# Performance work log

Hardware: AMD Instinct MI355X
Metric: run time of the kernel (lower is better)

The kernel has to match this reference:

```python
import jax, jax.numpy as jnp
import numpy as np

N = 50000          # nodes
E = 800000         # directed edges (before self loops)
H = 2              # attention heads
NEG_SLOPE = 0.2    # PyG GATv2 default
EPS = 1e-5         # GraphNorm eps
DIMS = [(3, 64), (64, 64), (64, 64)]


def _gatv2_layer(x, Wl, Wr, att, b, src, dst):
    # x: [N, din]; Wl, Wr: [din, H*C]; att: [H, C]; b: [C]
    n = x.shape[0]
    h, c = att.shape
    xl = (x @ Wl).reshape(n, h, c)   # source-side transform
    xr = (x @ Wr).reshape(n, h, c)   # target-side transform
    # edge-wise GATv2 score: a . leaky_relu(xl[j] + xr[i])
    e = jax.nn.leaky_relu(xl[src] + xr[dst], NEG_SLOPE)      # [E, H, C]
    logit = jnp.einsum('ehc,hc->eh', e, att)                 # [E, H]
    # segment softmax over incoming edges of each target node
    m = jax.ops.segment_max(logit, dst, num_segments=n)      # [N, H]
    a = jnp.exp(logit - m[dst])
    z = jax.ops.segment_sum(a, dst, num_segments=n)
    alpha = a / z[dst]                                       # [E, H]
    out = jax.ops.segment_sum(alpha[:, :, None] * xl[src], dst, num_segments=n)  # [N, H, C]
    return out.mean(axis=1) + b                              # concat=False -> head mean


def _graph_norm(x, w, b, ms):
    # single-graph GraphNorm: x -> w * (x - ms*mean) / sqrt(var + eps) + b
    mu = x.mean(axis=0)
    o = x - ms * mu
    var = (o * o).mean(axis=0)
    return w * o * jax.lax.rsqrt(var + EPS) + b


def setup_inputs() -> dict:
    key = jax.random.key(0)
    ks = jax.random.split(key, 2 + 3 * len(DIMS))
    inp = {
        'x': jax.random.normal(ks[0], (N, 3), dtype=jnp.float32),
        'edge_index': jax.random.randint(ks[1], (2, E), 0, N, dtype=jnp.int32),
    }
    for i, (din, dout) in enumerate(DIMS, start=1):
        k0, k1, k2 = ks[2 + 3 * (i - 1):2 + 3 * i]
        s_in = np.float32(1.0 / np.sqrt(din))
        s_att = np.float32(1.0 / np.sqrt(dout))
        inp[f'Wl{i}'] = jax.random.normal(k0, (din, H * dout), dtype=jnp.float32) * s_in
        inp[f'Wr{i}'] = jax.random.normal(k1, (din, H * dout), dtype=jnp.float32) * s_in
        inp[f'att{i}'] = jax.random.normal(k2, (H, dout), dtype=jnp.float32) * s_att
        inp[f'b{i}'] = jnp.zeros((dout,), dtype=jnp.float32)
        inp[f'gw{i}'] = jnp.ones((dout,), dtype=jnp.float32)
        inp[f'gb{i}'] = jnp.zeros((dout,), dtype=jnp.float32)
        inp[f'gm{i}'] = jnp.ones((dout,), dtype=jnp.float32)
    return inp


def reference(x, edge_index,
              Wl1, Wr1, att1, b1, gw1, gb1, gm1,
              Wl2, Wr2, att2, b2, gw2, gb2, gm2,
              Wl3, Wr3, att3, b3, gw3, gb3, gm3):
    n = x.shape[0]
    loop = jnp.arange(n, dtype=edge_index.dtype)
    src = jnp.concatenate([edge_index[0], loop])  # add_self_loops=True
    dst = jnp.concatenate([edge_index[1], loop])
    layers = [(Wl1, Wr1, att1, b1, gw1, gb1, gm1),
              (Wl2, Wr2, att2, b2, gw2, gb2, gm2),
              (Wl3, Wr3, att3, b3, gw3, gb3, gm3)]
    for Wl, Wr, att, b, gw, gb, gm in layers:
        x = _gatv2_layer(x, Wl, Wr, att, b, src, dst)
        x = jax.nn.relu(_graph_norm(x, gw, gb, gm))
    return x
```

## Files before the change

### kernel.cpp

```cpp
#include <hip/hip_runtime.h>
#include <math.h>

#define NN 50000
#define NE 800000
#define TE (NE + NN)
#define HC 128
#define NEG_SLOPE 0.2f
#define EPSV 1e-5f
#define NBUCK 64
#define GGRID 782
#define WTB 128
#define ZB 52
#define ZERO_N4 18644

typedef __attribute__((ext_vector_type(8))) short bf16x8;
typedef __attribute__((ext_vector_type(4))) float f32x4;
union BfU { uint4 u; bf16x8 b; };

__device__ __forceinline__ unsigned short f2bf(float x) {
    unsigned u = __float_as_uint(x);
    unsigned r = (u + 0x7fff + ((u >> 16) & 1)) >> 16;
    return (unsigned short)r;
}


__global__ __launch_bounds__(256) void count_k(const int* __restrict__ dst,
                                               int* __restrict__ cnt,
                                               int* __restrict__ rank) {
    int e = blockIdx.x * 256 + threadIdx.x;
    if (e >= TE) return;
    int d = (e < NE) ? dst[e] : (e - NE);
    rank[e] = atomicAdd(&cnt[d], 1);
}

__global__ __launch_bounds__(1024) void scan1_k(const int* __restrict__ cnt,
                                                int* __restrict__ excl,
                                                int* __restrict__ aux) {
    __shared__ int wsum[16];
    int tid = threadIdx.x;
    int gid = blockIdx.x * 1024 + tid;
    int lane = tid & 63, wid = tid >> 6;
    int v = (gid < NN) ? cnt[gid] : 0;
    int x = v;
#pragma unroll
    for (int off = 1; off < 64; off <<= 1) {
        int t = __shfl_up(x, off, 64);
        if (lane >= off) x += t;
    }
    if (lane == 63) wsum[wid] = x;
    __syncthreads();
    if (wid == 0 && lane < 16) {
        int y = wsum[lane];
#pragma unroll
        for (int off = 1; off < 16; off <<= 1) {
            int t = __shfl_up(y, off, 64);
            if (lane >= off) y += t;
        }
        wsum[lane] = y;
    }
    __syncthreads();
    int base = (wid > 0) ? wsum[wid - 1] : 0;
    int incl = base + x;
    if (gid < NN) excl[gid] = incl - v;
    if (tid == 1023) aux[blockIdx.x] = incl;
}

__global__ __launch_bounds__(256) void scatter_k(const int* __restrict__ srcp,
                                                 const int* __restrict__ dstp,
                                                 const int* __restrict__ excl,
                                                 const int* __restrict__ aux,
                                                 const int* __restrict__ rank,
                                                 int* __restrict__ row_ptr,
                                                 int* __restrict__ col,
                                                 int nblk) {
    __shared__ int auxs[64];
    if (threadIdx.x < 64) {
        int lane = threadIdx.x;
        int v = (lane < nblk) ? aux[lane] : 0;
        int x = v;
#pragma unroll
        for (int off = 1; off < 64; off <<= 1) {
            int t = __shfl_up(x, off, 64);
            if (lane >= off) x += t;
        }
        auxs[lane] = x - v;
    }
    __syncthreads();
    int e = blockIdx.x * 256 + threadIdx.x;
    if (e >= TE) return;
    if (e <= NN) row_ptr[e] = (e == NN) ? TE : excl[e] + auxs[e >> 10];
    int s, d;
    if (e < NE) { s = srcp[e]; d = dstp[e]; } else { s = e - NE; d = s; }
    col[excl[d] + auxs[d >> 10] + rank[e]] = s << 8;
}

__device__ __forceinline__ void store_xlp(char* xlp, int row, int c0, const float* a) {
    unsigned hsel = (unsigned)c0 >> 6;
    unsigned dd = (unsigned)c0 & 31;
    unsigned sub = (c0 & 32) ? 2u : 0u;
    char* q = xlp + (size_t)row * 256 + hsel * 128 + 4 * dd + sub;
#pragma unroll
    for (int j = 0; j < 4; ++j)
        *(unsigned short*)(q + 4 * j) = f2bf(a[j]);
}


__global__ __launch_bounds__(256) void init_k(const float* __restrict__ x,
                                              const float* __restrict__ Wl1,
                                              const float* __restrict__ Wr1,
                                              char* __restrict__ xlp,
                                              char* __restrict__ xrp,
                                              const float* __restrict__ Wl2,
                                              const float* __restrict__ Wr2,
                                              const float* __restrict__ Wl3,
                                              const float* __restrict__ Wr3,
                                              unsigned short* __restrict__ wt2,
                                              unsigned short* __restrict__ wt3,
                                              float4* __restrict__ zero4) {
    __shared__ float xs[32][72];
    __shared__ float ws[32][260];
    int b = blockIdx.x;
    int tid = threadIdx.x;

    if (b >= GGRID) {
        if (b < GGRID + WTB) {
            int idx = (b - GGRID) * 256 + tid;
            int l = idx >> 14;
            int rem = idx & 16383;
            int k = rem >> 8;
            int c = rem & 255;
            const float* W = (l == 0) ? (c < 128 ? Wl2 : Wr2) : (c < 128 ? Wl3 : Wr3);
            float v = W[k * 128 + (c & 127)];
            unsigned short* wt = (l == 0) ? wt2 : wt3;
            wt[c * 64 + k] = f2bf(v);
        } else {
            float4 zv; zv.x = zv.y = zv.z = zv.w = 0.f;
            for (int i = (b - GGRID - WTB) * 256 + tid; i < ZERO_N4; i += ZB * 256)
                zero4[i] = zv;
        }
        return;
    }

    int row0 = b * 64;
    int row_t = (tid >> 5) * 8;
    int c0 = (tid & 31) * 4;
    const int K = 3;

    float acc0[8][4];
    float acc1[8][4];
#pragma unroll
    for (int i = 0; i < 8; ++i)
#pragma unroll
        for (int j = 0; j < 4; ++j) { acc0[i][j] = 0.f; acc1[i][j] = 0.f; }

    for (int i = tid; i < 64 * K; i += 256) {
        int r = i / K;
        int k = i - r * K;
        int row = row0 + r;
        xs[k][r] = (row < NN) ? x[(size_t)row * K + k] : 0.f;
    }
    for (int i = tid; i < K * 64; i += 256) {
        int k = i >> 6;
        int cq = i & 63;
        const float* srcp = (cq < 32) ? &Wl1[(size_t)k * 128 + cq * 4]
                                      : &Wr1[(size_t)k * 128 + (cq - 32) * 4];
        float4 v = *(const float4*)srcp;
        *(float4*)&ws[k][cq * 4] = v;
    }
    __syncthreads();
    for (int k = 0; k < K; ++k) {
        float4 a0 = *(float4*)&xs[k][row_t];
        float4 a1 = *(float4*)&xs[k][row_t + 4];
        float4 b0 = *(float4*)&ws[k][c0];
        float4 b1 = *(float4*)&ws[k][c0 + 128];
        float av[8] = {a0.x, a0.y, a0.z, a0.w, a1.x, a1.y, a1.z, a1.w};
        float bl[4] = {b0.x, b0.y, b0.z, b0.w};
        float br[4] = {b1.x, b1.y, b1.z, b1.w};
#pragma unroll
        for (int i = 0; i < 8; ++i)
#pragma unroll
            for (int j = 0; j < 4; ++j) {
                acc0[i][j] += av[i] * bl[j];
                acc1[i][j] += av[i] * br[j];
            }
    }
#pragma unroll
    for (int i = 0; i < 8; ++i) {
        int row = row0 + row_t + i;
        if (row < NN) {
            store_xlp(xlp, row, c0, acc0[i]);
            store_xlp(xrp, row, c0, acc1[i]);
        }
    }
}

__device__ __forceinline__ void reduce_stats(const float* __restrict__ stats,
                                             const float* __restrict__ gw,
                                             const float* __restrict__ gb,
                                             const float* __restrict__ gm,
                                             float (*part)[128],
                                             float* __restrict__ cf_out) {
    int tid = threadIdx.x;
    int w = tid >> 6;
    int lane = tid & 63;
    float s = 0.f, s2 = 0.f;
    for (int b = 16 * w; b < 16 * w + 16; ++b) {
        s += stats[b * 128 + lane];
        s2 += stats[b * 128 + 64 + lane];
    }
    part[w][lane] = s;
    part[w][64 + lane] = s2;
    __syncthreads();
    if (tid < 64) {
        int c = tid;
        float sum = (part[0][c] + part[1][c]) + (part[2][c] + part[3][c]);
        float sum2 = (part[0][64 + c] + part[1][64 + c]) + (part[2][64 + c] + part[3][64 + c]);
        float inv_n = 1.f / (float)NN;
        float mu = sum * inv_n;
        float ex2 = sum2 * inv_n;
        float g = gm[c];
        float var = ex2 - 2.f * g * mu * mu + g * g * mu * mu;
        float rs = rsqrtf(var + EPSV);
        cf_out[c] = gw[c] * rs;
        cf_out[64 + c] = gb[c] - gw[c] * rs * g * mu;
    }
    __syncthreads();
}


__global__ __launch_bounds__(256) void gemm_mfma(const unsigned* __restrict__ hbf,
                                                 const float* __restrict__ stats,
                                                 const float* __restrict__ gw,
                                                 const float* __restrict__ gb,
                                                 const float* __restrict__ gm,
                                                 const unsigned short* __restrict__ wt,
                                                 char* __restrict__ xlp,
                                                 char* __restrict__ xrp,
                                                 int n) {
    __shared__ unsigned short xs[64][72];
    __shared__ float part[4][128];
    __shared__ float cfS[128];
    int tid = threadIdx.x;
    int row0 = blockIdx.x * 64;

    reduce_stats(stats, gw, gb, gm, part, cfS);

    {
        int r = tid >> 2;
        int q = tid & 3;
        int row = row0 + r;
        unsigned pk[8];
        if (row < n) {
            const unsigned* hp = hbf + (size_t)row * 32 + (q & 1) * 16;
            uint4 u0 = *(const uint4*)(hp + 0);
            uint4 u1 = *(const uint4*)(hp + 4);
            uint4 u2 = *(const uint4*)(hp + 8);
            uint4 u3 = *(const uint4*)(hp + 12);
            unsigned hv[16] = {u0.x, u0.y, u0.z, u0.w, u1.x, u1.y, u1.z, u1.w,
                               u2.x, u2.y, u2.z, u2.w, u3.x, u3.y, u3.z, u3.w};
            bool hi = (q >> 1) != 0;
#pragma unroll
            for (int i = 0; i < 4; ++i) {
                float4 v;
                v.x = hi ? __uint_as_float(hv[4 * i + 0] & 0xffff0000u) : __uint_as_float(hv[4 * i + 0] << 16);
                v.y = hi ? __uint_as_float(hv[4 * i + 1] & 0xffff0000u) : __uint_as_float(hv[4 * i + 1] << 16);
                v.z = hi ? __uint_as_float(hv[4 * i + 2] & 0xffff0000u) : __uint_as_float(hv[4 * i + 2] << 16);
                v.w = hi ? __uint_as_float(hv[4 * i + 3] & 0xffff0000u) : __uint_as_float(hv[4 * i + 3] << 16);
                float4 cw = *(const float4*)&cfS[q * 16 + 4 * i];
                float4 cb = *(const float4*)&cfS[64 + q * 16 + 4 * i];
                float r0 = fmaxf(fmaf(cw.x, v.x, cb.x), 0.f);
                float r1 = fmaxf(fmaf(cw.y, v.y, cb.y), 0.f);
                float r2 = fmaxf(fmaf(cw.z, v.z, cb.z), 0.f);
                float r3 = fmaxf(fmaf(cw.w, v.w, cb.w), 0.f);
                pk[2 * i]     = (unsigned)f2bf(r0) | ((unsigned)f2bf(r1) << 16);
                pk[2 * i + 1] = (unsigned)f2bf(r2) | ((unsigned)f2bf(r3) << 16);
            }
        } else {
#pragma unroll
            for (int i = 0; i < 8; ++i) pk[i] = 0;
        }
        uint4* dst = (uint4*)&xs[r][q * 16];
        dst[0] = make_uint4(pk[0], pk[1], pk[2], pk[3]);
        dst[1] = make_uint4(pk[4], pk[5], pk[6], pk[7]);
    }
    __syncthreads();

    int w = tid >> 6;
    int lane = tid & 63;
    int m = lane & 15;
    int quad = lane >> 4;

    BfU a0, a1;
    a0.u = *(const uint4*)&xs[16 * w + m][quad * 8];
    a1.u = *(const uint4*)&xs[16 * w + m][32 + quad * 8];

    const char* wtb = (const char*)wt + (size_t)(m * 128 + quad * 16);

    f32x4 acc[16];
#pragma unroll
    for (int c = 0; c < 16; ++c) acc[c] = (f32x4){0.f, 0.f, 0.f, 0.f};
#pragma unroll
    for (int c = 0; c < 16; ++c) {
        BfU b0, b1;
        b0.u = *(const uint4*)(wtb + c * 2048);
        b1.u = *(const uint4*)(wtb + c * 2048 + 64);
        acc[c] = __builtin_amdgcn_mfma_f32_16x16x32_bf16(a0.b, b0.b, acc[c], 0, 0, 0);
        acc[c] = __builtin_amdgcn_mfma_f32_16x16x32_bf16(a1.b, b1.b, acc[c], 0, 0, 0);
    }

    int rbase = row0 + 16 * w + quad * 4;
#pragma unroll
    for (int pi = 0; pi < 4; ++pi) {
        int c = (pi & 1) + (pi >> 1) * 4;
        int head = pi >> 1;
        int dd = (pi & 1) * 16 + m;
#pragma unroll
        for (int r = 0; r < 4; ++r) {
            int row = rbase + r;
            if (row < n) {
                unsigned vl = (unsigned)f2bf(acc[c][r]) | ((unsigned)f2bf(acc[c + 2][r]) << 16);
                unsigned vr = (unsigned)f2bf(acc[c + 8][r]) | ((unsigned)f2bf(acc[c + 10][r]) << 16);
                *(unsigned*)(xlp + (size_t)row * 256 + head * 128 + 4 * dd) = vl;
                *(unsigned*)(xrp + (size_t)row * 256 + head * 128 + 4 * dd) = vr;
            }
        }
    }
}


__device__ __forceinline__ void unpack8(uint4 q, float* l) {
    l[0] = __uint_as_float(q.x << 16);
    l[1] = __uint_as_float(q.x & 0xffff0000u);
    l[2] = __uint_as_float(q.y << 16);
    l[3] = __uint_as_float(q.y & 0xffff0000u);
    l[4] = __uint_as_float(q.z << 16);
    l[5] = __uint_as_float(q.z & 0xffff0000u);
    l[6] = __uint_as_float(q.w << 16);
    l[7] = __uint_as_float(q.w & 0xffff0000u);
}

__device__ __forceinline__ float logit_part(const float* l, const float* xv, const float* av) {
    float u1 = 0.f, u2 = 0.f;
#pragma unroll
    for (int k = 0; k < 8; ++k) {
        float t = l[k] + xv[k];
        u1 = fmaf(av[k], t, u1);
        u2 = fmaf(av[k], fabsf(t), u2);
    }
    return fmaf(0.6f, u1, 0.4f * u2);
}

__device__ __forceinline__ float head_reduce(float w) {
    w += __shfl_xor(w, 1, 64);
    w += __shfl_xor(w, 2, 64);
    w += __shfl_xor(w, 4, 64);
    return w;
}

__device__ __forceinline__ void attn_pair(const char* __restrict__ xlp, int lp16,
                                          int off0, int off1, bool v0, bool v1,
                                          const float* xv, const float* av,
                                          float* o, float& zacc) {
    uint4 q0 = *(const uint4*)(xlp + (unsigned)(off0 + lp16));
    uint4 q1 = *(const uint4*)(xlp + (unsigned)(off1 + lp16));
    float l0[8], l1[8];
    unpack8(q0, l0);
    unpack8(q1, l1);
    float w0 = head_reduce(logit_part(l0, xv, av));
    float w1 = head_reduce(logit_part(l1, xv, av));
    float e0 = __expf(w0);
    float e1 = __expf(w1);
    if (!v0) e0 = 0.f;
    if (!v1) e1 = 0.f;
    zacc += e0 + e1;
#pragma unroll
    for (int k = 0; k < 8; ++k) o[k] = fmaf(e1, l1[k], fmaf(e0, l0[k], o[k]));
}

__device__ __forceinline__ void attn_quad(const char* __restrict__ xlp, int lp16,
                                          int off0, int off1, int off2, int off3,
                                          const float* xv, const float* av,
                                          float* o, float& zacc) {
    uint4 q0 = *(const uint4*)(xlp + (unsigned)(off0 + lp16));
    uint4 q1 = *(const uint4*)(xlp + (unsigned)(off1 + lp16));
    uint4 q2 = *(const uint4*)(xlp + (unsigned)(off2 + lp16));
    uint4 q3 = *(const uint4*)(xlp + (unsigned)(off3 + lp16));
    float l0[8], l1[8], l2[8], l3[8];
    unpack8(q0, l0);
    unpack8(q1, l1);
    unpack8(q2, l2);
    unpack8(q3, l3);
    float w0 = head_reduce(logit_part(l0, xv, av));
    float w1 = head_reduce(logit_part(l1, xv, av));
    float w2 = head_reduce(logit_part(l2, xv, av));
    float w3 = head_reduce(logit_part(l3, xv, av));
    float e0 = __expf(w0);
    float e1 = __expf(w1);
    float e2 = __expf(w2);
    float e3 = __expf(w3);
    zacc += (e0 + e1) + (e2 + e3);
#pragma unroll
    for (int k = 0; k < 8; ++k)
        o[k] = fmaf(e3, l3[k], fmaf(e2, l2[k], fmaf(e1, l1[k], fmaf(e0, l0[k], o[k]))));
}

__global__ __launch_bounds__(256) void attn_k(const char* __restrict__ xlp,
                                              const char* __restrict__ xrp,
                                              const float* __restrict__ att,
                                              const float* __restrict__ bias,
                                              const int* __restrict__ row_ptr,
                                              const int* __restrict__ coloff,
                                              unsigned* __restrict__ hout,
                                              float* __restrict__ stats) {
    __shared__ float sb[4][64];
    int tid = threadIdx.x;
    int lane = tid & 63;
    int wv = tid >> 6;
    int node = blockIdx.x * 4 + wv;
    int t16 = lane & 15;
    int slot = (lane >> 4) * 2;
    int head = t16 >> 3;
    int dd = (t16 & 7) * 4;
    int lp16 = t16 * 16;
    int cbase = head * 64 + dd;

    float xv[8];
    unpack8(*(const uint4*)(xrp + ((size_t)node << 8) + lp16), xv);
    float4 a0 = *(const float4*)(att + cbase);
    float4 a1 = *(const float4*)(att + cbase + 32);
    float av[8] = {a0.x, a1.x, a0.y, a1.y, a0.z, a1.z, a0.w, a1.w};

    float o[8];
#pragma unroll
    for (int k = 0; k < 8; ++k) o[k] = 0.f;
    float zacc = 0.f;

    int beg = __builtin_amdgcn_readfirstlane(row_ptr[node]);
    int end = __builtin_amdgcn_readfirstlane(row_ptr[node + 1]);

    int idx = beg;
    for (; idx + 16 <= end; idx += 16) {
        int off0 = coloff[idx + slot];
        int off1 = coloff[idx + slot + 1];
        int off2 = coloff[idx + 8 + slot];
        int off3 = coloff[idx + 8 + slot + 1];
        attn_quad(xlp, lp16, off0, off1, off2, off3, xv, av, o, zacc);
    }
    if (idx + 8 <= end) {
        int off0 = coloff[idx + slot];
        int off1 = coloff[idx + slot + 1];
        attn_pair(xlp, lp16, off0, off1, true, true, xv, av, o, zacc);
        idx += 8;
    }
    if (idx < end) {
        int e1 = end - 1;
        int i0 = idx + slot, i1 = idx + slot + 1;
        int off0 = coloff[min(i0, e1)];
        int off1 = coloff[min(i1, e1)];
        attn_pair(xlp, lp16, off0, off1, i0 < end, i1 < end, xv, av, o, zacc);
    }

    float z = zacc + __shfl_xor(zacc, 16, 64);
    z += __shfl_xor(z, 32, 64);
    float zi = 1.0f / z;
    float r[8];
#pragma unroll
    for (int k = 0; k < 8; ++k) {
        float v = o[k] + __shfl_xor(o[k], 16, 64);
        v += __shfl_xor(v, 32, 64);
        v *= zi;
        float p = __shfl_xor(v, 8, 64);
        r[k] = 0.5f * (v + p);
    }
    if (lane < 8) {
        float4 b0 = *(const float4*)(bias + dd);
        float4 b1 = *(const float4*)(bias + dd + 32);
        float rl0 = r[0] + b0.x, rl1 = r[2] + b0.y, rl2 = r[4] + b0.z, rl3 = r[6] + b0.w;
        float rh0 = r[1] + b1.x, rh1 = r[3] + b1.y, rh2 = r[5] + b1.z, rh3 = r[7] + b1.w;
        unsigned pk0 = (unsigned)f2bf(rl0) | ((unsigned)f2bf(rh0) << 16);
        unsigned pk1 = (unsigned)f2bf(rl1) | ((unsigned)f2bf(rh1) << 16);
        unsigned pk2 = (unsigned)f2bf(rl2) | ((unsigned)f2bf(rh2) << 16);
        unsigned pk3 = (unsigned)f2bf(rl3) | ((unsigned)f2bf(rh3) << 16);
        *(uint4*)&hout[(size_t)node * 32 + dd] = make_uint4(pk0, pk1, pk2, pk3);
        *(float4*)&sb[wv][dd] = make_float4(rl0, rl1, rl2, rl3);
        *(float4*)&sb[wv][dd + 32] = make_float4(rh0, rh1, rh2, rh3);
    }
    __syncthreads();
    if (tid < 64) {
        int c = tid;
        float v0 = sb[0][c], v1 = sb[1][c], v2 = sb[2][c], v3 = sb[3][c];
        float s = (v0 + v1) + (v2 + v3);
        float s2 = fmaf(v0, v0, v1 * v1) + fmaf(v2, v2, v3 * v3);
        float* bkt = stats + (size_t)(blockIdx.x & (NBUCK - 1)) * 128;
        atomicAdd(&bkt[c], s);
        atomicAdd(&bkt[64 + c], s2);
    }
}


__global__ __launch_bounds__(256) void apply_k(const unsigned* __restrict__ h,
                                               const float* __restrict__ stats,
                                               const float* __restrict__ gw,
                                               const float* __restrict__ gb,
                                               const float* __restrict__ gm,
                                               float* __restrict__ y) {
    __shared__ float part[4][128];
    __shared__ float cfS[128];
    reduce_stats(stats, gw, gb, gm, part, cfS);

    int i = blockIdx.x * 256 + threadIdx.x;
    if (i >= NN * 8) return;
    int node = i >> 3;
    int j = (i & 7) * 4;
    uint4 u = *(const uint4*)(h + (size_t)node * 32 + j);
    float4 lo, hi;
    lo.x = __uint_as_float(u.x << 16); hi.x = __uint_as_float(u.x & 0xffff0000u);
    lo.y = __uint_as_float(u.y << 16); hi.y = __uint_as_float(u.y & 0xffff0000u);
    lo.z = __uint_as_float(u.z << 16); hi.z = __uint_as_float(u.z & 0xffff0000u);
    lo.w = __uint_as_float(u.w << 16); hi.w = __uint_as_float(u.w & 0xffff0000u);
    float4 cwl = *(const float4*)&cfS[j];
    float4 cbl = *(const float4*)&cfS[64 + j];
    float4 cwh = *(const float4*)&cfS[32 + j];
    float4 cbh = *(const float4*)&cfS[96 + j];
    float4 rl, rh;
    rl.x = fmaxf(fmaf(cwl.x, lo.x, cbl.x), 0.f);
    rl.y = fmaxf(fmaf(cwl.y, lo.y, cbl.y), 0.f);
    rl.z = fmaxf(fmaf(cwl.z, lo.z, cbl.z), 0.f);
    rl.w = fmaxf(fmaf(cwl.w, lo.w, cbl.w), 0.f);
    rh.x = fmaxf(fmaf(cwh.x, hi.x, cbh.x), 0.f);
    rh.y = fmaxf(fmaf(cwh.y, hi.y, cbh.y), 0.f);
    rh.z = fmaxf(fmaf(cwh.z, hi.z, cbh.z), 0.f);
    rh.w = fmaxf(fmaf(cwh.w, hi.w, cbh.w), 0.f);
    *(float4*)&y[(size_t)node * 64 + j] = rl;
    *(float4*)&y[(size_t)node * 64 + 32 + j] = rh;
}


extern "C" void kernel_launch(void* const* d_in, const int* in_sizes, int n_in,
                              void* d_out, int out_size, void* d_ws, size_t ws_size,
                              hipStream_t stream) {
    const float* x0 = (const float*)d_in[0];
    const int* ei = (const int*)d_in[1];
    const int* srcp = ei;
    const int* dstp = ei + NE;

    const float* Wl[3], *Wr[3], *att[3], *bv[3], *gw[3], *gb[3], *gm[3];
    for (int l = 0; l < 3; ++l) {
        int base = 2 + 7 * l;
        Wl[l] = (const float*)d_in[base + 0];
        Wr[l] = (const float*)d_in[base + 1];
        att[l] = (const float*)d_in[base + 2];
        bv[l] = (const float*)d_in[base + 3];
        gw[l] = (const float*)d_in[base + 4];
        gb[l] = (const float*)d_in[base + 5];
        gm[l] = (const float*)d_in[base + 6];
    }

    char* p = (char*)d_ws;
    auto take = [&](size_t bytes) -> void* {
        void* r = (void*)p;
        p += (bytes + 255) & ~(size_t)255;
        return r;
    };
    char* xlp = (char*)take((size_t)NN * 256);
    char* xrp = (char*)take((size_t)NN * 256);
    unsigned* hb = (unsigned*)take((size_t)NN * 32 * 4);
    char* zr = (char*)take(298304);
    float* stats = (float*)zr;
    int* cnt = (int*)(zr + 98304);
    int* excl = (int*)take((size_t)NN * 4);
    int* row_ptr = (int*)take((size_t)(NN + 1) * 4);
    int* rank = (int*)take((size_t)TE * 4);
    int* col = (int*)take((size_t)TE * 4);
    int* aux = (int*)take(64 * 4);
    unsigned short* wt2 = (unsigned short*)take(16384 * 2);
    unsigned short* wt3 = (unsigned short*)take(16384 * 2);

    int nblk = (NN + 1023) / 1024;
    int egrid = (TE + 255) / 256;

    init_k<<<GGRID + WTB + ZB, 256, 0, stream>>>(x0, Wl[0], Wr[0], xlp, xrp,
                                                 Wl[1], Wr[1], Wl[2], Wr[2],
                                                 wt2, wt3, (float4*)zr);
    count_k<<<egrid, 256, 0, stream>>>(dstp, cnt, rank);
    scan1_k<<<nblk, 1024, 0, stream>>>(cnt, excl, aux);
    scatter_k<<<egrid, 256, 0, stream>>>(srcp, dstp, excl, aux, rank, row_ptr, col, nblk);

    int ggrid = (NN + 63) / 64;
    int agrid = NN / 4;
    for (int l = 0; l < 3; ++l) {
        if (l > 0)
            gemm_mfma<<<ggrid, 256, 0, stream>>>(hb, stats + (size_t)(l - 1) * NBUCK * 128,
                                                 gw[l - 1], gb[l - 1], gm[l - 1],
                                                 (l == 1) ? wt2 : wt3, xlp, xrp, NN);
        attn_k<<<agrid, 256, 0, stream>>>(xlp, xrp, att[l], bv[l], row_ptr, col, hb,
                                          stats + (size_t)l * NBUCK * 128);
    }
    apply_k<<<(NN * 8 + 255) / 256, 256, 0, stream>>>(hb, stats + (size_t)2 * NBUCK * 128,
                                                      gw[2], gb[2], gm[2], (float*)d_out);
}
```

Baseline: 358.1 us.

## Remap attention lanes to 8 per edge with DPP reductions and prefetched offsets

```diff
diff --git a/kernel.cpp b/kernel.cpp
--- a/kernel.cpp
+++ b/kernel.cpp
@@ -328,80 +328,43 @@
 }
 
 
-__device__ __forceinline__ void unpack8(uint4 q, float* l) {
-    l[0] = __uint_as_float(q.x << 16);
-    l[1] = __uint_as_float(q.x & 0xffff0000u);
-    l[2] = __uint_as_float(q.y << 16);
-    l[3] = __uint_as_float(q.y & 0xffff0000u);
-    l[4] = __uint_as_float(q.z << 16);
-    l[5] = __uint_as_float(q.z & 0xffff0000u);
-    l[6] = __uint_as_float(q.w << 16);
-    l[7] = __uint_as_float(q.w & 0xffff0000u);
-}
-
-__device__ __forceinline__ float logit_part(const float* l, const float* xv, const float* av) {
+__device__ __forceinline__ float quad_reduce(float x) {
+    x += __int_as_float(__builtin_amdgcn_mov_dpp(__float_as_int(x), 0xB1, 0xF, 0xF, true));
+    x += __int_as_float(__builtin_amdgcn_mov_dpp(__float_as_int(x), 0x4E, 0xF, 0xF, true));
+    return x;
+}
+
+__device__ __forceinline__ float ror8_add(float x) {
+    return x + __int_as_float(__builtin_amdgcn_mov_dpp(__float_as_int(x), 0x128, 0xF, 0xF, true));
+}
+
+__device__ __forceinline__ void unpack16(uint4 q0, uint4 q1, float* l) {
+    unsigned u[8] = {q0.x, q0.y, q0.z, q0.w, q1.x, q1.y, q1.z, q1.w};
+#pragma unroll
+    for (int j = 0; j < 8; ++j) {
+        l[2 * j]     = __uint_as_float(u[j] << 16);
+        l[2 * j + 1] = __uint_as_float(u[j] & 0xffff0000u);
+    }
+}
+
+__device__ __forceinline__ void edge_proc(uint4 q0, uint4 q1, bool valid,
+                                          const float* xv, const float* av,
+                                          float* o, float& zacc) {
+    float l[16];
+    unpack16(q0, q1, l);
     float u1 = 0.f, u2 = 0.f;
 #pragma unroll
-    for (int k = 0; k < 8; ++k) {
+    for (int k = 0; k < 16; ++k) {
         float t = l[k] + xv[k];
         u1 = fmaf(av[k], t, u1);
         u2 = fmaf(av[k], fabsf(t), u2);
     }
-    return fmaf(0.6f, u1, 0.4f * u2);
-}
-
-__device__ __forceinline__ float head_reduce(float w) {
-    w += __shfl_xor(w, 1, 64);
-    w += __shfl_xor(w, 2, 64);
-    w += __shfl_xor(w, 4, 64);
-    return w;
-}
-
-__device__ __forceinline__ void attn_pair(const char* __restrict__ xlp, int lp16,
-                                          int off0, int off1, bool v0, bool v1,
-                                          const float* xv, const float* av,
-                                          float* o, float& zacc) {
-    uint4 q0 = *(const uint4*)(xlp + (unsigned)(off0 + lp16));
-    uint4 q1 = *(const uint4*)(xlp + (unsigned)(off1 + lp16));
-    float l0[8], l1[8];
-    unpack8(q0, l0);
-    unpack8(q1, l1);
-    float w0 = head_reduce(logit_part(l0, xv, av));
-    float w1 = head_reduce(logit_part(l1, xv, av));
-    float e0 = __expf(w0);
-    float e1 = __expf(w1);
-    if (!v0) e0 = 0.f;
-    if (!v1) e1 = 0.f;
-    zacc += e0 + e1;
-#pragma unroll
-    for (int k = 0; k < 8; ++k) o[k] = fmaf(e1, l1[k], fmaf(e0, l0[k], o[k]));
-}
-
-__device__ __forceinline__ void attn_quad(const char* __restrict__ xlp, int lp16,
-                                          int off0, int off1, int off2, int off3,
-                                          const float* xv, const float* av,
-                                          float* o, float& zacc) {
-    uint4 q0 = *(const uint4*)(xlp + (unsigned)(off0 + lp16));
-    uint4 q1 = *(const uint4*)(xlp + (unsigned)(off1 + lp16));
-    uint4 q2 = *(const uint4*)(xlp + (unsigned)(off2 + lp16));
-    uint4 q3 = *(const uint4*)(xlp + (unsigned)(off3 + lp16));
-    float l0[8], l1[8], l2[8], l3[8];
-    unpack8(q0, l0);
-    unpack8(q1, l1);
-    unpack8(q2, l2);
-    unpack8(q3, l3);
-    float w0 = head_reduce(logit_part(l0, xv, av));
-    float w1 = head_reduce(logit_part(l1, xv, av));
-    float w2 = head_reduce(logit_part(l2, xv, av));
-    float w3 = head_reduce(logit_part(l3, xv, av));
-    float e0 = __expf(w0);
-    float e1 = __expf(w1);
-    float e2 = __expf(w2);
-    float e3 = __expf(w3);
-    zacc += (e0 + e1) + (e2 + e3);
-#pragma unroll
-    for (int k = 0; k < 8; ++k)
-        o[k] = fmaf(e3, l3[k], fmaf(e2, l2[k], fmaf(e1, l1[k], fmaf(e0, l0[k], o[k]))));
+    float w = quad_reduce(fmaf(0.6f, u1, 0.4f * u2));
+    float e = __expf(w);
+    if (!valid) e = 0.f;
+    zacc += e;
+#pragma unroll
+    for (int k = 0; k < 16; ++k) o[k] = fmaf(e, l[k], o[k]);
 }
 
 __global__ __launch_bounds__(256) void attn_k(const char* __restrict__ xlp,
@@ -417,73 +380,111 @@
     int lane = tid & 63;
     int wv = tid >> 6;
     int node = blockIdx.x * 4 + wv;
-    int t16 = lane & 15;
-    int slot = (lane >> 4) * 2;
-    int head = t16 >> 3;
-    int dd = (t16 & 7) * 4;
-    int lp16 = t16 * 16;
-    int cbase = head * 64 + dd;
-
-    float xv[8];
-    unpack8(*(const uint4*)(xrp + ((size_t)node << 8) + lp16), xv);
-    float4 a0 = *(const float4*)(att + cbase);
-    float4 a1 = *(const float4*)(att + cbase + 32);
-    float av[8] = {a0.x, a1.x, a0.y, a1.y, a0.z, a1.z, a0.w, a1.w};
-
-    float o[8];
-#pragma unroll
-    for (int k = 0; k < 8; ++k) o[k] = 0.f;
+    int g = lane >> 3;
+    int t8 = lane & 7;
+    int b32 = t8 * 32;
+    int hd = t8 >> 2;
+    int dd = (t8 & 3) * 8;
+
+    float xv[16];
+    {
+        const char* xq = xrp + ((size_t)node << 8) + b32;
+        unpack16(*(const uint4*)xq, *(const uint4*)(xq + 16), xv);
+    }
+    float av[16];
+    {
+        int base = hd * 64 + dd;
+        float4 a0 = *(const float4*)(att + base);
+        float4 a1 = *(const float4*)(att + base + 4);
+        float4 c0 = *(const float4*)(att + base + 32);
+        float4 c1 = *(const float4*)(att + base + 36);
+        av[0] = a0.x;  av[1] = c0.x;  av[2] = a0.y;  av[3] = c0.y;
+        av[4] = a0.z;  av[5] = c0.z;  av[6] = a0.w;  av[7] = c0.w;
+        av[8] = a1.x;  av[9] = c1.x;  av[10] = a1.y; av[11] = c1.y;
+        av[12] = a1.z; av[13] = c1.z; av[14] = a1.w; av[15] = c1.w;
+    }
+
+    float o[16];
+#pragma unroll
+    for (int k = 0; k < 16; ++k) o[k] = 0.f;
     float zacc = 0.f;
 
     int beg = __builtin_amdgcn_readfirstlane(row_ptr[node]);
     int end = __builtin_amdgcn_readfirstlane(row_ptr[node + 1]);
+    int e1 = end - 1;
 
     int idx = beg;
-    for (; idx + 16 <= end; idx += 16) {
-        int off0 = coloff[idx + slot];
-        int off1 = coloff[idx + slot + 1];
-        int off2 = coloff[idx + 8 + slot];
-        int off3 = coloff[idx + 8 + slot + 1];
-        attn_quad(xlp, lp16, off0, off1, off2, off3, xv, av, o, zacc);
+    if (idx + 16 <= end) {
+        int offA = coloff[idx + g];
+        int offB = coloff[idx + 8 + g];
+        for (;;) {
+            const char* pa = xlp + (unsigned)(offA + b32);
+            const char* pb = xlp + (unsigned)(offB + b32);
+            uint4 qa0 = *(const uint4*)pa;
+            uint4 qa1 = *(const uint4*)(pa + 16);
+            uint4 qb0 = *(const uint4*)pb;
+            uint4 qb1 = *(const uint4*)(pb + 16);
+            idx += 16;
+            bool more = (idx + 16 <= end);
+            int nA = coloff[more ? idx + g : e1];
+            int nB = coloff[more ? idx + 8 + g : e1];
+            edge_proc(qa0, qa1, true, xv, av, o, zacc);
+            edge_proc(qb0, qb1, true, xv, av, o, zacc);
+            offA = nA; offB = nB;
+            if (!more) break;
+        }
     }
     if (idx + 8 <= end) {
-        int off0 = coloff[idx + slot];
-        int off1 = coloff[idx + slot + 1];
-        attn_pair(xlp, lp16, off0, off1, true, true, xv, av, o, zacc);
+        int off = coloff[idx + g];
+        const char* pa = xlp + (unsigned)(off + b32);
+        uint4 q0 = *(const uint4*)pa;
+        uint4 q1 = *(const uint4*)(pa + 16);
+        edge_proc(q0, q1, true, xv, av, o, zacc);
         idx += 8;
     }
     if (idx < end) {
-        int e1 = end - 1;
-        int i0 = idx + slot, i1 = idx + slot + 1;
-        int off0 = coloff[min(i0, e1)];
-        int off1 = coloff[min(i1, e1)];
-        attn_pair(xlp, lp16, off0, off1, i0 < end, i1 < end, xv, av, o, zacc);
-    }
-
-    float z = zacc + __shfl_xor(zacc, 16, 64);
+        int i0 = idx + g;
+        int off = coloff[min(i0, e1)];
+        const char* pa = xlp + (unsigned)(off + b32);
+        uint4 q0 = *(const uint4*)pa;
+        uint4 q1 = *(const uint4*)(pa + 16);
+        edge_proc(q0, q1, i0 < end, xv, av, o, zacc);
+    }
+
+    float z = ror8_add(zacc);
+    z += __shfl_xor(z, 16, 64);
     z += __shfl_xor(z, 32, 64);
     float zi = 1.0f / z;
-    float r[8];
-#pragma unroll
-    for (int k = 0; k < 8; ++k) {
-        float v = o[k] + __shfl_xor(o[k], 16, 64);
+    float r[16];
+#pragma unroll
+    for (int k = 0; k < 16; ++k) {
+        float v = ror8_add(o[k]);
+        v += __shfl_xor(v, 16, 64);
         v += __shfl_xor(v, 32, 64);
         v *= zi;
-        float p = __shfl_xor(v, 8, 64);
-        r[k] = 0.5f * (v + p);
-    }
-    if (lane < 8) {
-        float4 b0 = *(const float4*)(bias + dd);
-        float4 b1 = *(const float4*)(bias + dd + 32);
-        float rl0 = r[0] + b0.x, rl1 = r[2] + b0.y, rl2 = r[4] + b0.z, rl3 = r[6] + b0.w;
-        float rh0 = r[1] + b1.x, rh1 = r[3] + b1.y, rh2 = r[5] + b1.z, rh3 = r[7] + b1.w;
-        unsigned pk0 = (unsigned)f2bf(rl0) | ((unsigned)f2bf(rh0) << 16);
-        unsigned pk1 = (unsigned)f2bf(rl1) | ((unsigned)f2bf(rh1) << 16);
-        unsigned pk2 = (unsigned)f2bf(rl2) | ((unsigned)f2bf(rh2) << 16);
-        unsigned pk3 = (unsigned)f2bf(rl3) | ((unsigned)f2bf(rh3) << 16);
-        *(uint4*)&hout[(size_t)node * 32 + dd] = make_uint4(pk0, pk1, pk2, pk3);
-        *(float4*)&sb[wv][dd] = make_float4(rl0, rl1, rl2, rl3);
-        *(float4*)&sb[wv][dd + 32] = make_float4(rh0, rh1, rh2, rh3);
+        float pq = __shfl_xor(v, 4, 64);
+        r[k] = 0.5f * (v + pq);
+    }
+    if (lane < 4) {
+        int ddl = lane * 8;
+        float4 b0 = *(const float4*)(bias + ddl);
+        float4 b1 = *(const float4*)(bias + ddl + 4);
+        float4 c0 = *(const float4*)(bias + ddl + 32);
+        float4 c1 = *(const float4*)(bias + ddl + 36);
+        float bl[8] = {b0.x, b0.y, b0.z, b0.w, b1.x, b1.y, b1.z, b1.w};
+        float bh[8] = {c0.x, c0.y, c0.z, c0.w, c1.x, c1.y, c1.z, c1.w};
+        unsigned pk[8];
+#pragma unroll
+        for (int j = 0; j < 8; ++j) {
+            float rl = r[2 * j] + bl[j];
+            float rh = r[2 * j + 1] + bh[j];
+            pk[j] = (unsigned)f2bf(rl) | ((unsigned)f2bf(rh) << 16);
+            sb[wv][ddl + j] = rl;
+            sb[wv][ddl + 32 + j] = rh;
+        }
+        uint4* dst = (uint4*)&hout[(size_t)node * 32 + ddl];
+        dst[0] = make_uint4(pk[0], pk[1], pk[2], pk[3]);
+        dst[1] = make_uint4(pk[4], pk[5], pk[6], pk[7]);
     }
     __syncthreads();
     if (tid < 64) {
```

Measured after the change: 373.1 us. +4.2%, slower.
